# Optimization experiments

Measured on AMD Instinct MI355X. Metric: run time of the kernel, lower is better.

The kernel has to match this reference:

```python
import jax, jax.numpy as jnp
import numpy as np

PATCH, WIN = 3, 7


def _unfold(x, k):
    # torch F.unfold(x, k, padding=k//2), stride 1 -> [b, c, k*k, h, w]
    # channel-major ordering (c slowest, then kernel row, then kernel col)
    pad = k // 2
    b, c, h, w = x.shape
    xp = jnp.pad(x, ((0, 0), (0, 0), (pad, pad), (pad, pad)))
    return jnp.stack([xp[:, :, i:i + h, j:j + w]
                      for i in range(k) for j in range(k)], axis=2)


def _conv3(x, w, b=None):
    y = jax.lax.conv_general_dilated(x, w, (1, 1), [(1, 1), (1, 1)],
                                     dimension_numbers=('NCHW', 'OIHW', 'NCHW'))
    if b is not None:
        y = y + b[None, :, None, None]
    return y


def _head(u_feat, pan_feat, w_phi, w_theta, w_g, p, ws):
    # SelfAttention: windowed/patch neighborhood attention
    b, c, h, w = pan_feat.shape
    phi = jnp.einsum('oi,bihw->bohw', w_phi, pan_feat)
    theta = jnp.einsum('oi,bihw->bohw', w_theta, pan_feat)
    thp = _unfold(theta, p).reshape(b, c * p * p, h, w)        # [b,D,h,w]
    php = _unfold(phi, p).reshape(b, c * p * p, h, w)          # [b,D,h,w]
    phw = _unfold(php, ws)                                     # [b,D,K,h,w], K=ws*ws
    att = jax.nn.softmax(jnp.einsum('bdhw,bdkhw->bhwk', thp, phw), axis=-1)
    g = jnp.einsum('oi,bihw->bohw', w_g, u_feat)
    gw = _unfold(g, ws)                                        # [b,cu,K,h,w]
    return jnp.einsum('bhwk,bckhw->bchw', att, gw)


def _forward(u, pan, w_nlu, w_nlpan, g_phi, g_theta, g_g, s_phi, s_theta, s_g,
             m_phi, m_theta, m_g, mlp_w, mlp_b, w_resu, w_respan,
             rb0_w1, rb0_b1, rb0_w2, rb0_b2, rb1_w1, rb1_b1, rb1_w2, rb1_b2,
             rb2_w1, rb2_b1, rb2_w2, rb2_b2, w_recon):
    uf = _conv3(u, w_nlu)      # [b,5,h,w]
    pf = _conv3(pan, w_nlpan)  # [b,3,h,w]
    h1 = _head(uf, pf, g_phi, g_theta, g_g, PATCH, WIN)
    h2 = _head(uf, uf, s_phi, s_theta, s_g, 1, WIN)
    h3 = _head(uf, jnp.concatenate([uf, pf], axis=1), m_phi, m_theta, m_g, PATCH, WIN)
    # mlp: Linear(3,1) over stacked heads (last dim of size 3)
    att = h1 * mlp_w[0, 0] + h2 * mlp_w[0, 1] + h3 * mlp_w[0, 2] + mlp_b[0]
    ru = _conv3(u, w_resu)
    rp = _conv3(pan, w_respan)
    x = jnp.concatenate([att, ru, rp], axis=1)  # [b, fc+10, h, w]
    rbs = [(rb0_w1, rb0_b1, rb0_w2, rb0_b2),
           (rb1_w1, rb1_b1, rb1_w2, rb1_b2),
           (rb2_w1, rb2_b1, rb2_w2, rb2_b2)]
    for w1, b1, w2, b2 in rbs:
        f = jax.nn.relu(_conv3(x, w1, b1))
        f = _conv3(f, w2, b2)
        x = jax.nn.relu(f + x)
    return _conv3(x, w_recon)


def setup_inputs() -> dict:
    key = jax.random.key(0)
    ks = jax.random.split(key, 32)
    def n(i, shape, s=0.1):
        return jax.random.normal(ks[i], shape, dtype=jnp.float32) * s
    B, H, W = 1, 128, 128
    FC = 32
    C = FC + 10
    inp = {
        'u': jax.random.normal(ks[0], (B, 8, H, W), dtype=jnp.float32),
        'pan': jax.random.normal(ks[1], (B, 1, H, W), dtype=jnp.float32),
        'w_nlu': n(2, (5, 8, 3, 3)),
        'w_nlpan': n(3, (3, 1, 3, 3)),
        'g_phi': n(4, (3, 3)), 'g_theta': n(5, (3, 3)), 'g_g': n(6, (5, 5)),
        's_phi': n(7, (5, 5)), 's_theta': n(8, (5, 5)), 's_g': n(9, (5, 5)),
        'm_phi': n(10, (8, 8)), 'm_theta': n(11, (8, 8)), 'm_g': n(12, (5, 5)),
        'mlp_w': n(13, (1, 3), 0.5), 'mlp_b': n(14, (1,), 0.1),
        'w_resu': n(15, (FC, 8, 3, 3)), 'w_respan': n(16, (5, 1, 3, 3)),
        'w_recon': n(17, (8, C, 3, 3)),
    }
    k = 18
    for i in range(3):
        inp[f'rb{i}_w1'] = n(k, (C, C, 3, 3))
        inp[f'rb{i}_b1'] = n(k + 1, (C,), 0.01)
        inp[f'rb{i}_w2'] = n(k + 2, (C, C, 3, 3))
        inp[f'rb{i}_b2'] = n(k + 3, (C,), 0.01)
        k += 4
    return inp


def reference(u, pan, w_nlu, w_nlpan, g_phi, g_theta, g_g, s_phi, s_theta, s_g,
              m_phi, m_theta, m_g, mlp_w, mlp_b, w_resu, w_respan,
              rb0_w1, rb0_b1, rb0_w2, rb0_b2, rb1_w1, rb1_b1, rb1_w2, rb1_b2,
              rb2_w1, rb2_b1, rb2_w2, rb2_b2, w_recon):
    return _forward(u, pan, w_nlu, w_nlpan, g_phi, g_theta, g_g, s_phi, s_theta,
                    s_g, m_phi, m_theta, m_g, mlp_w, mlp_b, w_resu, w_respan,
                    rb0_w1, rb0_b1, rb0_w2, rb0_b2, rb1_w1, rb1_b1, rb1_w2,
                    rb1_b2, rb2_w1, rb2_b1, rb2_w2, rb2_b2, w_recon)
```

## Files before the change

kernel.cpp:

```cpp
#include <hip/hip_runtime.h>


#define DEV __device__ __forceinline__
typedef float f32x4 __attribute__((ext_vector_type(4)));
typedef __bf16 bf16x8 __attribute__((ext_vector_type(8)));
typedef unsigned short u16;
typedef unsigned int u32;

constexpr int N = 128 * 128;

constexpr int OFF_PHI1 =   0 * N;
constexpr int OFF_TH1  =   3 * N;
constexpr int OFF_PHI2 =   6 * N;
constexpr int OFF_TH2  =  11 * N;
constexpr int OFF_PHI3 =  16 * N;
constexpr int OFF_TH3  =  24 * N;
constexpr int OFF_G1   =  32 * N;
constexpr int OFF_G2   =  37 * N;
constexpr int OFF_G3   =  42 * N;
constexpr int OFF_X    =  47 * N;
constexpr int OFF_OH1  =  89 * N;
constexpr int OFF_OH2  =  94 * N;
constexpr int OFF_OH3  =  99 * N;
constexpr int XPLANE   = 130 * 136;
constexpr int OFF_XPAD = 110 * N;
constexpr int OFF_FPAD = 133 * N;
constexpr int OFF_SLAB = 156 * N;
constexpr int OFF_BTAB = 160 * N;
constexpr int SLAB_RB  = 18432;
constexpr int SLAB_RC  = 110592;
constexpr int SLAB_TOT = 116736;
constexpr int ZPB      = 528;
constexpr int ZTOT     = 2 * 42 * ZPB;
constexpr int WPREP_TOT = 384 + SLAB_TOT + ZTOT;

DEV bool inb(int y, int x) { return (unsigned)y < 128u && (unsigned)x < 128u; }
DEV u16 f2bf(float f) {
    unsigned u = __float_as_uint(f);
    return (u16)((u + 0x7fffu + ((u >> 16) & 1u)) >> 16);
}

__global__ __launch_bounds__(256, 2) void features_k(
    const float* __restrict__ u, const float* __restrict__ pan,
    const float* __restrict__ wnlu, const float* __restrict__ wnlpan,
    const float* __restrict__ gphi, const float* __restrict__ gth,
    const float* __restrict__ gg, const float* __restrict__ sphi,
    const float* __restrict__ sth, const float* __restrict__ sg,
    const float* __restrict__ mphi, const float* __restrict__ mth,
    const float* __restrict__ mg, float* __restrict__ ws) {
    const int p = blockIdx.x * 256 + threadIdx.x;
    const int y = p >> 7, x = p & 127;

    float uv[8][9];
#pragma unroll
    for (int ic = 0; ic < 8; ++ic)
#pragma unroll
        for (int i = 0; i < 3; ++i)
#pragma unroll
            for (int j = 0; j < 3; ++j) {
                int yy = y + i - 1, xx = x + j - 1;
                uv[ic][i * 3 + j] = inb(yy, xx) ? u[ic * N + yy * 128 + xx] : 0.f;
            }

    float uf[5] = {0, 0, 0, 0, 0};
#pragma unroll
    for (int ic = 0; ic < 8; ++ic)
#pragma unroll
        for (int k = 0; k < 9; ++k)
#pragma unroll
            for (int o = 0; o < 5; ++o)
                uf[o] = fmaf(uv[ic][k], wnlu[(o * 8 + ic) * 9 + k], uf[o]);

    if (blockIdx.y == 0) {
#pragma unroll
        for (int o = 0; o < 5; ++o) {
            float a = 0, b = 0, c1 = 0, c2 = 0, c3 = 0;
#pragma unroll
            for (int i = 0; i < 5; ++i) {
                a  = fmaf(sphi[o * 5 + i], uf[i], a);
                b  = fmaf(sth [o * 5 + i], uf[i], b);
                c1 = fmaf(gg  [o * 5 + i], uf[i], c1);
                c2 = fmaf(sg  [o * 5 + i], uf[i], c2);
                c3 = fmaf(mg  [o * 5 + i], uf[i], c3);
            }
            ws[OFF_PHI2 + o * N + p] = a;
            ws[OFF_TH2  + o * N + p] = b;
            ws[OFF_G1   + o * N + p] = c1;
            ws[OFF_G2   + o * N + p] = c2;
            ws[OFF_G3   + o * N + p] = c3;
        }
    } else {
        float pv[9];
#pragma unroll
        for (int i = 0; i < 3; ++i)
#pragma unroll
            for (int j = 0; j < 3; ++j) {
                int yy = y + i - 1, xx = x + j - 1;
                pv[i * 3 + j] = inb(yy, xx) ? pan[yy * 128 + xx] : 0.f;
            }
        float pf[3] = {0, 0, 0};
#pragma unroll
        for (int k = 0; k < 9; ++k)
#pragma unroll
            for (int o = 0; o < 3; ++o)
                pf[o] = fmaf(pv[k], wnlpan[o * 9 + k], pf[o]);

        float cat[8] = {uf[0], uf[1], uf[2], uf[3], uf[4], pf[0], pf[1], pf[2]};
#pragma unroll
        for (int o = 0; o < 3; ++o) {
            float a = 0, b = 0;
#pragma unroll
            for (int i = 0; i < 3; ++i) {
                a = fmaf(gphi[o * 3 + i], pf[i], a);
                b = fmaf(gth [o * 3 + i], pf[i], b);
            }
            ws[OFF_PHI1 + o * N + p] = a;
            ws[OFF_TH1  + o * N + p] = b;
        }
#pragma unroll
        for (int o = 0; o < 8; ++o) {
            float a = 0, b = 0;
#pragma unroll
            for (int i = 0; i < 8; ++i) {
                a = fmaf(mphi[o * 8 + i], cat[i], a);
                b = fmaf(mth [o * 8 + i], cat[i], b);
            }
            ws[OFF_PHI3 + o * N + p] = a;
            ws[OFF_TH3  + o * N + p] = b;
        }
    }
}

template <int C, int P>
DEV void head_tile(const float* __restrict__ phi, const float* __restrict__ theta,
                   const float* __restrict__ g, float* __restrict__ oh,
                   float* __restrict__ smem, int ty0, int tx0, int t) {
    constexpr int PR  = P / 2;
    constexpr int H3  = 3 + PR;
    constexpr int W   = 6 + P;
    constexpr int TTH = 8 + 2 * PR, TTW = 16 + 2 * PR;
    constexpr int PTH = 8 + 2 * H3, PTW = 16 + 2 * H3;
    constexpr int GTH = 14, GTW = 22;

    float* sT = smem;
    float* sP = sT + C * TTH * TTW;
    float* sG = sP + C * PTH * PTW;

#pragma unroll
    for (int c = 0; c < C; ++c)
#pragma unroll
        for (int base = 0; base < TTH * TTW; base += 256) {
            int i = base + t;
            if (i < TTH * TTW) {
                int r = i / TTW, cc = i - r * TTW;
                int gy = ty0 - PR + r, gx = tx0 - PR + cc;
                sT[c * TTH * TTW + i] =
                    inb(gy, gx) ? theta[c * N + gy * 128 + gx] : 0.f;
            }
        }
#pragma unroll
    for (int c = 0; c < C; ++c)
#pragma unroll
        for (int base = 0; base < PTH * PTW; base += 256) {
            int i = base + t;
            if (i < PTH * PTW) {
                int r = i / PTW, cc = i - r * PTW;
                int gy = ty0 - H3 + r, gx = tx0 - H3 + cc;
                sP[c * PTH * PTW + i] =
                    inb(gy, gx) ? phi[c * N + gy * 128 + gx] : 0.f;
            }
        }
#pragma unroll
    for (int c = 0; c < 5; ++c)
#pragma unroll
        for (int base = 0; base < GTH * GTW; base += 256) {
            int i = base + t;
            if (i < GTH * GTW) {
                int r = i / GTW, cc = i - r * GTW;
                int gy = ty0 - 3 + r, gx = tx0 - 3 + cc;
                sG[c * GTH * GTW + i] =
                    inb(gy, gx) ? g[c * N + gy * 128 + gx] : 0.f;
            }
        }
    __syncthreads();

    const int wave = t >> 6, lane = t & 63, m = lane >> 5;
    const int pidx = (lane & 31) | (wave << 5);
    const int py = pidx >> 4, px = pidx & 15;
    const int gy = ty0 + py, gx = tx0 + px;
    const int dbase = m * 3;

    float s[28];
#pragma unroll
    for (int k = 0; k < 28; ++k) s[k] = 0.f;

    for (int c = 0; c < C; ++c) {
        const float* tc = sT + c * TTH * TTW;
        const float* pc = sP + c * PTH * PTW;
        float T[P][P];
#pragma unroll
        for (int i = 0; i < P; ++i)
#pragma unroll
            for (int j = 0; j < P; ++j)
                T[i][j] = tc[(py + i) * TTW + px + j];
        float R[P][W];
#pragma unroll
        for (int r = 0; r < P; ++r)
#pragma unroll
            for (int w = 0; w < W; ++w)
                R[r][w] = pc[(py + dbase + r) * PTW + px + w];
#pragma unroll
        for (int dd = 0; dd < 4; ++dd) {
#pragma unroll
            for (int dx = 0; dx < 7; ++dx) {
                float a = 0.f;
#pragma unroll
                for (int i = 0; i < P; ++i)
#pragma unroll
                    for (int j = 0; j < P; ++j)
                        a = fmaf(T[i][j], R[i][dx + j], a);
                s[dd * 7 + dx] += a;
            }
            if (dd < 3) {
#pragma unroll
                for (int r = 0; r < P - 1; ++r)
#pragma unroll
                    for (int w = 0; w < W; ++w) R[r][w] = R[r + 1][w];
                int row = py + dbase + dd + P;
#pragma unroll
                for (int w = 0; w < W; ++w)
                    R[P - 1][w] = pc[row * PTW + px + w];
            }
        }
    }
#pragma unroll
    for (int k = 0; k < 28; ++k) {
        int d = dbase + k / 7, dx = k % 7;
        if (!inb(gy + d - 3, gx + dx - 3)) s[k] = 0.f;
    }
    const bool half0 = (m == 0);
    float mx = -3.0e38f;
#pragma unroll
    for (int k = 0; k < 28; ++k) {
        bool own = half0 || (k >= 7);
        mx = own ? fmaxf(mx, s[k]) : mx;
    }
    mx = fmaxf(mx, __shfl_xor(mx, 32));
    float sum = 0.f;
#pragma unroll
    for (int k = 0; k < 28; ++k) {
        bool own = half0 || (k >= 7);
        float e = own ? __expf(s[k] - mx) : 0.f;
        s[k] = e;
        sum += e;
    }
    sum += __shfl_xor(sum, 32);

    float o[5] = {0, 0, 0, 0, 0};
#pragma unroll
    for (int k = 0; k < 28; ++k) {
        int d = dbase + k / 7, dx = k % 7;
        int gr = (py + d) * GTW + px + dx;
#pragma unroll
        for (int c5 = 0; c5 < 5; ++c5)
            o[c5] = fmaf(s[k], sG[c5 * GTH * GTW + gr], o[c5]);
    }
#pragma unroll
    for (int c5 = 0; c5 < 5; ++c5) o[c5] += __shfl_xor(o[c5], 32);

    if (half0) {
        float inv = 1.f / sum;
        int p = gy * 128 + gx;
#pragma unroll
        for (int c5 = 0; c5 < 5; ++c5) oh[c5 * N + p] = o[c5] * inv;
    }
}

__global__ __launch_bounds__(256) void heads_k(float* __restrict__ ws) {
    __shared__ float smem[6052];
    const int t = threadIdx.x;
    const int ty0 = (blockIdx.x >> 3) * 8, tx0 = (blockIdx.x & 7) * 16;
    if (blockIdx.y == 0)
        head_tile<3, 3>(ws + OFF_PHI1, ws + OFF_TH1, ws + OFF_G1, ws + OFF_OH1,
                        smem, ty0, tx0, t);
    else if (blockIdx.y == 1)
        head_tile<5, 1>(ws + OFF_PHI2, ws + OFF_TH2, ws + OFF_G2, ws + OFF_OH2,
                        smem, ty0, tx0, t);
    else
        head_tile<8, 3>(ws + OFF_PHI3, ws + OFF_TH3, ws + OFF_G3, ws + OFF_OH3,
                        smem, ty0, tx0, t);
}

struct WPtrs { const float* w[7]; };

__global__ __launch_bounds__(256) void wprep_k(WPtrs wp, u16* __restrict__ slab,
                                               u16* __restrict__ btab,
                                               u16* __restrict__ xpad,
                                               u16* __restrict__ fpad) {
    int idx = blockIdx.x * 256 + threadIdx.x;
    if (idx >= WPREP_TOT) return;
    if (idx < 384) {
        u16 v = 0;
        if (idx < 378) {
            int ic = idx / 9, tau = idx - ic * 9;
            v = (u16)(ic * 216 + (tau / 3) * 72 + (tau % 3));
        }
        btab[idx] = v;
        return;
    }
    idx -= 384;
    if (idx < SLAB_TOT) {
        const float* W;
        int mt, ks, lane, j, ocv;
        if (idx < SLAB_RC) {
            int cv = idx / SLAB_RB, r = idx - cv * SLAB_RB;
            mt = r / 6144; r -= mt * 6144;
            ks = r / 512;  r -= ks * 512;
            lane = r / 8;  j = r - lane * 8;
            W = wp.w[cv]; ocv = 42;
        } else {
            int r = idx - SLAB_RC;
            mt = 0;
            ks = r / 512;  r -= ks * 512;
            lane = r / 8;  j = r - lane * 8;
            W = wp.w[6]; ocv = 8;
        }
        int k  = ks * 32 + (lane >> 4) * 8 + j;
        int oc = mt * 16 + (lane & 15);
        u16 v = 0;
        if (k < 378 && oc < ocv) {
            int ic = k / 9, tau = k - ic * 9;
            v = f2bf(W[(oc * 42 + ic) * 9 + tau]);
        }
        slab[idx] = v;
        return;
    }
    idx -= SLAB_TOT;
    u16* buf = (idx < 42 * ZPB) ? xpad : fpad;
    int e = (idx < 42 * ZPB) ? idx : idx - 42 * ZPB;
    int plane = e / ZPB, rem = e - plane * ZPB;
    int row, col;
    if (rem < 136)      { row = 0;             col = rem; }
    else if (rem < 272) { row = 129;           col = rem - 136; }
    else if (rem < 400) { row = 1 + rem - 272; col = 0; }
    else                { row = 1 + rem - 400; col = 129; }
    buf[plane * XPLANE + row * 136 + col] = 0;
}

__global__ __launch_bounds__(256, 2) void assemble_k(
    const float* __restrict__ u, const float* __restrict__ pan,
    const float* __restrict__ wres, const float* __restrict__ wrp,
    const float* __restrict__ mlpw, const float* __restrict__ mlpb,
    float* __restrict__ ws, u16* __restrict__ xpad) {
    const int p = blockIdx.x * 256 + threadIdx.x;
    const int y = p >> 7, x = p & 127;
    const int padp = (y + 1) * 136 + (x + 1);
    float* xb = ws + OFF_X;

    if (blockIdx.y == 0) {
        const float w0 = mlpw[0], w1 = mlpw[1], w2 = mlpw[2];
        const float bb = mlpb[0];
#pragma unroll
        for (int c = 0; c < 5; ++c) {
            float a = ws[OFF_OH1 + c * N + p] * w0 +
                      ws[OFF_OH2 + c * N + p] * w1 +
                      ws[OFF_OH3 + c * N + p] * w2 + bb;
            xb[c * N + p] = a;
            xpad[c * XPLANE + padp] = f2bf(a);
        }
        float pv[9];
#pragma unroll
        for (int i = 0; i < 3; ++i)
#pragma unroll
            for (int j = 0; j < 3; ++j) {
                int yy = y + i - 1, xx = x + j - 1;
                pv[i * 3 + j] = inb(yy, xx) ? pan[yy * 128 + xx] : 0.f;
            }
        float a5[5] = {0, 0, 0, 0, 0};
#pragma unroll
        for (int k = 0; k < 9; ++k)
#pragma unroll
            for (int o = 0; o < 5; ++o)
                a5[o] = fmaf(pv[k], wrp[o * 9 + k], a5[o]);
#pragma unroll
        for (int o = 0; o < 5; ++o) {
            xb[(37 + o) * N + p] = a5[o];
            xpad[(37 + o) * XPLANE + padp] = f2bf(a5[o]);
        }
    } else {
        const int ob = (blockIdx.y - 1) * 8;
        float uv[8][9];
#pragma unroll
        for (int ic = 0; ic < 8; ++ic)
#pragma unroll
            for (int i = 0; i < 3; ++i)
#pragma unroll
                for (int j = 0; j < 3; ++j) {
                    int yy = y + i - 1, xx = x + j - 1;
                    uv[ic][i * 3 + j] =
                        inb(yy, xx) ? u[ic * N + yy * 128 + xx] : 0.f;
                }
        float acc[8] = {0, 0, 0, 0, 0, 0, 0, 0};
#pragma unroll
        for (int ic = 0; ic < 8; ++ic)
#pragma unroll
            for (int k = 0; k < 9; ++k)
#pragma unroll
                for (int o = 0; o < 8; ++o)
                    acc[o] = fmaf(uv[ic][k], wres[((ob + o) * 8 + ic) * 9 + k],
                                  acc[o]);
#pragma unroll
        for (int o = 0; o < 8; ++o) {
            xb[(5 + ob + o) * N + p] = acc[o];
            xpad[(5 + ob + o) * XPLANE + padp] = f2bf(acc[o]);
        }
    }
}

template <int MT, int OCV, bool BIAS, bool RELU, bool SKIP, bool WF32, bool WPAD>
__global__ __launch_bounds__(256, 1) void convm_k(
    const u16* __restrict__ xin, const u16* __restrict__ slab,
    const u16* __restrict__ btab, const float* __restrict__ bs,
    const float* __restrict__ skip, float* __restrict__ of32,
    u16* __restrict__ opad) {
    __shared__ __align__(16) u16 sX[9072];
    __shared__ __align__(16) u16 sBt[384];
    const int t = threadIdx.x;
    const int y = blockIdx.x >> 1, x0 = (blockIdx.x & 1) << 6;

    const u16* srcbase = xin + y * 136 + x0;
#pragma unroll
    for (int it = 0; it < 4; ++it) {
        int c = it * 256 + t;
        if (c < 1008) {
            int row = c >> 3, slot = c & 7;
            int ic = row / 3, r = row - ic * 3;
            uint4 v = *((const uint4*)(srcbase + ic * XPLANE + r * 136) + slot);
            *(uint4*)(sX + row * 72 + slot * 8) = v;
        }
    }
    if (t < 126) {
        int ic = t / 3, r = t - ic * 3;
        u32 v = *(const u32*)(srcbase + ic * XPLANE + r * 136 + 64);
        *(u32*)(sX + t * 72 + 64) = v;
    }
    for (int i = t; i < 384; i += 256) sBt[i] = btab[i];
    __syncthreads();

    const int lane = t & 63, wave = t >> 6;
    const int quad = lane >> 4, col = lane & 15;
    const int ncol = wave * 16 + col;

    union AB { uint4 u; bf16x8 b; };
    AB a[MT][12];
#pragma unroll
    for (int mt = 0; mt < MT; ++mt)
#pragma unroll
        for (int ks = 0; ks < 12; ++ks)
            a[mt][ks].u = ((const uint4*)slab)[(mt * 12 + ks) * 64 + lane];

    f32x4 acc[MT];
#pragma unroll
    for (int mt = 0; mt < MT; ++mt) acc[mt] = {0.f, 0.f, 0.f, 0.f};

#pragma unroll
    for (int ks = 0; ks < 12; ++ks) {
        union { uint4 u; u16 s[8]; } off;
        off.u = *(const uint4*)(sBt + ks * 32 + quad * 8);
        union { u16 s[8]; bf16x8 b; } bv;
#pragma unroll
        for (int j = 0; j < 8; ++j) bv.s[j] = sX[off.s[j] + ncol];
#pragma unroll
        for (int mt = 0; mt < MT; ++mt)
            acc[mt] = __builtin_amdgcn_mfma_f32_16x16x32_bf16(
                a[mt][ks].b, bv.b, acc[mt], 0, 0, 0);
    }

    const int xg = x0 + ncol;
    const int px = y * 128 + xg;
    const int padp = (y + 1) * 136 + (xg + 1);
#pragma unroll
    for (int mt = 0; mt < MT; ++mt)
#pragma unroll
        for (int reg = 0; reg < 4; ++reg) {
            int oc = mt * 16 + quad * 4 + reg;
            if (oc < OCV) {
                float v = acc[mt][reg];
                if (BIAS) v += bs[oc];
                if (SKIP) v += skip[oc * N + px];
                if (RELU) v = fmaxf(v, 0.f);
                if (WF32) of32[oc * N + px] = v;
                if (WPAD) opad[oc * XPLANE + padp] = f2bf(v);
            }
        }
}

extern "C" void kernel_launch(void* const* d_in, const int* in_sizes, int n_in,
                              void* d_out, int out_size, void* d_ws, size_t ws_size,
                              hipStream_t stream) {
    (void)in_sizes; (void)n_in; (void)out_size; (void)ws_size;
    float* ws = (float*)d_ws;
    float* out = (float*)d_out;

    const float* u      = (const float*)d_in[0];
    const float* pan    = (const float*)d_in[1];
    const float* wnlu   = (const float*)d_in[2];
    const float* wnlpan = (const float*)d_in[3];
    const float* gphi   = (const float*)d_in[4];
    const float* gth    = (const float*)d_in[5];
    const float* gg     = (const float*)d_in[6];
    const float* sphi   = (const float*)d_in[7];
    const float* sth    = (const float*)d_in[8];
    const float* sg     = (const float*)d_in[9];
    const float* mphi   = (const float*)d_in[10];
    const float* mth    = (const float*)d_in[11];
    const float* mg     = (const float*)d_in[12];
    const float* mlpw   = (const float*)d_in[13];
    const float* mlpb   = (const float*)d_in[14];
    const float* wres   = (const float*)d_in[15];
    const float* wrp    = (const float*)d_in[16];
    const float* wrecon = (const float*)d_in[17];

    u16* xpad = (u16*)(ws + OFF_XPAD);
    u16* fpad = (u16*)(ws + OFF_FPAD);
    u16* slab = (u16*)(ws + OFF_SLAB);
    u16* btab = (u16*)(ws + OFF_BTAB);

    features_k<<<dim3(N / 256, 2), 256, 0, stream>>>(
        u, pan, wnlu, wnlpan, gphi, gth, gg, sphi, sth, sg, mphi, mth, mg, ws);
    heads_k<<<dim3(128, 3), 256, 0, stream>>>(ws);

    WPtrs wp;
    wp.w[0] = (const float*)d_in[18]; wp.w[1] = (const float*)d_in[20];
    wp.w[2] = (const float*)d_in[22]; wp.w[3] = (const float*)d_in[24];
    wp.w[4] = (const float*)d_in[26]; wp.w[5] = (const float*)d_in[28];
    wp.w[6] = wrecon;
    wprep_k<<<(WPREP_TOT + 255) / 256, 256, 0, stream>>>(wp, slab, btab,
                                                         xpad, fpad);

    assemble_k<<<dim3(N / 256, 5), 256, 0, stream>>>(u, pan, wres, wrp, mlpw,
                                                     mlpb, ws, xpad);

    for (int r = 0; r < 3; ++r) {
        const float* b1 = (const float*)d_in[19 + 4 * r];
        const float* b2 = (const float*)d_in[21 + 4 * r];
        convm_k<3, 42, true, true, false, false, true>
            <<<256, 256, 0, stream>>>(xpad, slab + (2 * r) * SLAB_RB, btab, b1,
                                      nullptr, nullptr, fpad);
        convm_k<3, 42, true, true, true, true, true>
            <<<256, 256, 0, stream>>>(fpad, slab + (2 * r + 1) * SLAB_RB, btab,
                                      b2, ws + OFF_X, ws + OFF_X, xpad);
    }
    convm_k<1, 8, false, false, false, true, false>
        <<<256, 256, 0, stream>>>(xpad, slab + SLAB_RC, btab, nullptr, nullptr,
                                  out, nullptr);
}
```

Measured before the change: 210.5 us.

## Merge feature and weight prep kernels, shrink head and conv tiles for more blocks

Folds the feature projection kernel and the weight/slab preparation kernel into one launch, with block ranges split by blockIdx. Head attention tiles shrink from 8x16 to 8x8 pixels with 128-thread blocks, giving 768 blocks instead of 384. The MFMA conv kernels go from 64-pixel to 32-pixel row segments with 128 threads and 512 blocks, and the shared row stride and gather table change to match. The aim is fewer launches and more blocks across the many CUs, at the cost of more halo reloading per pixel and less reuse.

```diff
diff --git a/kernel.cpp b/kernel.cpp
--- a/kernel.cpp
+++ b/kernel.cpp
@@ -33,6 +33,7 @@
 constexpr int ZPB      = 528;
 constexpr int ZTOT     = 2 * 42 * ZPB;
 constexpr int WPREP_TOT = 384 + SLAB_TOT + ZTOT;
+constexpr int WPREP_BLK = (WPREP_TOT + 255) / 256;
 
 DEV bool inb(int y, int x) { return (unsigned)y < 128u && (unsigned)x < 128u; }
 DEV u16 f2bf(float f) {
@@ -40,270 +41,112 @@
     return (u16)((u + 0x7fffu + ((u >> 16) & 1u)) >> 16);
 }
 
-__global__ __launch_bounds__(256, 2) void features_k(
-    const float* __restrict__ u, const float* __restrict__ pan,
-    const float* __restrict__ wnlu, const float* __restrict__ wnlpan,
-    const float* __restrict__ gphi, const float* __restrict__ gth,
-    const float* __restrict__ gg, const float* __restrict__ sphi,
-    const float* __restrict__ sth, const float* __restrict__ sg,
-    const float* __restrict__ mphi, const float* __restrict__ mth,
-    const float* __restrict__ mg, float* __restrict__ ws) {
-    const int p = blockIdx.x * 256 + threadIdx.x;
-    const int y = p >> 7, x = p & 127;
-
-    float uv[8][9];
-#pragma unroll
-    for (int ic = 0; ic < 8; ++ic)
-#pragma unroll
-        for (int i = 0; i < 3; ++i)
-#pragma unroll
-            for (int j = 0; j < 3; ++j) {
-                int yy = y + i - 1, xx = x + j - 1;
-                uv[ic][i * 3 + j] = inb(yy, xx) ? u[ic * N + yy * 128 + xx] : 0.f;
-            }
-
-    float uf[5] = {0, 0, 0, 0, 0};
-#pragma unroll
-    for (int ic = 0; ic < 8; ++ic)
-#pragma unroll
-        for (int k = 0; k < 9; ++k)
-#pragma unroll
-            for (int o = 0; o < 5; ++o)
-                uf[o] = fmaf(uv[ic][k], wnlu[(o * 8 + ic) * 9 + k], uf[o]);
-
-    if (blockIdx.y == 0) {
-#pragma unroll
-        for (int o = 0; o < 5; ++o) {
-            float a = 0, b = 0, c1 = 0, c2 = 0, c3 = 0;
-#pragma unroll
-            for (int i = 0; i < 5; ++i) {
-                a  = fmaf(sphi[o * 5 + i], uf[i], a);
-                b  = fmaf(sth [o * 5 + i], uf[i], b);
-                c1 = fmaf(gg  [o * 5 + i], uf[i], c1);
-                c2 = fmaf(sg  [o * 5 + i], uf[i], c2);
-                c3 = fmaf(mg  [o * 5 + i], uf[i], c3);
-            }
-            ws[OFF_PHI2 + o * N + p] = a;
-            ws[OFF_TH2  + o * N + p] = b;
-            ws[OFF_G1   + o * N + p] = c1;
-            ws[OFF_G2   + o * N + p] = c2;
-            ws[OFF_G3   + o * N + p] = c3;
-        }
-    } else {
-        float pv[9];
-#pragma unroll
-        for (int i = 0; i < 3; ++i)
-#pragma unroll
-            for (int j = 0; j < 3; ++j) {
-                int yy = y + i - 1, xx = x + j - 1;
-                pv[i * 3 + j] = inb(yy, xx) ? pan[yy * 128 + xx] : 0.f;
-            }
-        float pf[3] = {0, 0, 0};
-#pragma unroll
-        for (int k = 0; k < 9; ++k)
-#pragma unroll
-            for (int o = 0; o < 3; ++o)
-                pf[o] = fmaf(pv[k], wnlpan[o * 9 + k], pf[o]);
-
-        float cat[8] = {uf[0], uf[1], uf[2], uf[3], uf[4], pf[0], pf[1], pf[2]};
-#pragma unroll
-        for (int o = 0; o < 3; ++o) {
-            float a = 0, b = 0;
-#pragma unroll
-            for (int i = 0; i < 3; ++i) {
-                a = fmaf(gphi[o * 3 + i], pf[i], a);
-                b = fmaf(gth [o * 3 + i], pf[i], b);
-            }
-            ws[OFF_PHI1 + o * N + p] = a;
-            ws[OFF_TH1  + o * N + p] = b;
-        }
-#pragma unroll
-        for (int o = 0; o < 8; ++o) {
-            float a = 0, b = 0;
-#pragma unroll
-            for (int i = 0; i < 8; ++i) {
-                a = fmaf(mphi[o * 8 + i], cat[i], a);
-                b = fmaf(mth [o * 8 + i], cat[i], b);
-            }
-            ws[OFF_PHI3 + o * N + p] = a;
-            ws[OFF_TH3  + o * N + p] = b;
-        }
-    }
-}
-
-template <int C, int P>
-DEV void head_tile(const float* __restrict__ phi, const float* __restrict__ theta,
-                   const float* __restrict__ g, float* __restrict__ oh,
-                   float* __restrict__ smem, int ty0, int tx0, int t) {
-    constexpr int PR  = P / 2;
-    constexpr int H3  = 3 + PR;
-    constexpr int W   = 6 + P;
-    constexpr int TTH = 8 + 2 * PR, TTW = 16 + 2 * PR;
-    constexpr int PTH = 8 + 2 * H3, PTW = 16 + 2 * H3;
-    constexpr int GTH = 14, GTW = 22;
-
-    float* sT = smem;
-    float* sP = sT + C * TTH * TTW;
-    float* sG = sP + C * PTH * PTW;
-
-#pragma unroll
-    for (int c = 0; c < C; ++c)
-#pragma unroll
-        for (int base = 0; base < TTH * TTW; base += 256) {
-            int i = base + t;
-            if (i < TTH * TTW) {
-                int r = i / TTW, cc = i - r * TTW;
-                int gy = ty0 - PR + r, gx = tx0 - PR + cc;
-                sT[c * TTH * TTW + i] =
-                    inb(gy, gx) ? theta[c * N + gy * 128 + gx] : 0.f;
-            }
-        }
-#pragma unroll
-    for (int c = 0; c < C; ++c)
-#pragma unroll
-        for (int base = 0; base < PTH * PTW; base += 256) {
-            int i = base + t;
-            if (i < PTH * PTW) {
-                int r = i / PTW, cc = i - r * PTW;
-                int gy = ty0 - H3 + r, gx = tx0 - H3 + cc;
-                sP[c * PTH * PTW + i] =
-                    inb(gy, gx) ? phi[c * N + gy * 128 + gx] : 0.f;
-            }
-        }
-#pragma unroll
-    for (int c = 0; c < 5; ++c)
-#pragma unroll
-        for (int base = 0; base < GTH * GTW; base += 256) {
-            int i = base + t;
-            if (i < GTH * GTW) {
-                int r = i / GTW, cc = i - r * GTW;
-                int gy = ty0 - 3 + r, gx = tx0 - 3 + cc;
-                sG[c * GTH * GTW + i] =
-                    inb(gy, gx) ? g[c * N + gy * 128 + gx] : 0.f;
-            }
-        }
-    __syncthreads();
-
-    const int wave = t >> 6, lane = t & 63, m = lane >> 5;
-    const int pidx = (lane & 31) | (wave << 5);
-    const int py = pidx >> 4, px = pidx & 15;
-    const int gy = ty0 + py, gx = tx0 + px;
-    const int dbase = m * 3;
-
-    float s[28];
-#pragma unroll
-    for (int k = 0; k < 28; ++k) s[k] = 0.f;
-
-    for (int c = 0; c < C; ++c) {
-        const float* tc = sT + c * TTH * TTW;
-        const float* pc = sP + c * PTH * PTW;
-        float T[P][P];
-#pragma unroll
-        for (int i = 0; i < P; ++i)
-#pragma unroll
-            for (int j = 0; j < P; ++j)
-                T[i][j] = tc[(py + i) * TTW + px + j];
-        float R[P][W];
-#pragma unroll
-        for (int r = 0; r < P; ++r)
-#pragma unroll
-            for (int w = 0; w < W; ++w)
-                R[r][w] = pc[(py + dbase + r) * PTW + px + w];
-#pragma unroll
-        for (int dd = 0; dd < 4; ++dd) {
-#pragma unroll
-            for (int dx = 0; dx < 7; ++dx) {
-                float a = 0.f;
-#pragma unroll
-                for (int i = 0; i < P; ++i)
-#pragma unroll
-                    for (int j = 0; j < P; ++j)
-                        a = fmaf(T[i][j], R[i][dx + j], a);
-                s[dd * 7 + dx] += a;
-            }
-            if (dd < 3) {
-#pragma unroll
-                for (int r = 0; r < P - 1; ++r)
-#pragma unroll
-                    for (int w = 0; w < W; ++w) R[r][w] = R[r + 1][w];
-                int row = py + dbase + dd + P;
-#pragma unroll
-                for (int w = 0; w < W; ++w)
-                    R[P - 1][w] = pc[row * PTW + px + w];
-            }
-        }
-    }
-#pragma unroll
-    for (int k = 0; k < 28; ++k) {
-        int d = dbase + k / 7, dx = k % 7;
-        if (!inb(gy + d - 3, gx + dx - 3)) s[k] = 0.f;
-    }
-    const bool half0 = (m == 0);
-    float mx = -3.0e38f;
-#pragma unroll
-    for (int k = 0; k < 28; ++k) {
-        bool own = half0 || (k >= 7);
-        mx = own ? fmaxf(mx, s[k]) : mx;
-    }
-    mx = fmaxf(mx, __shfl_xor(mx, 32));
-    float sum = 0.f;
-#pragma unroll
-    for (int k = 0; k < 28; ++k) {
-        bool own = half0 || (k >= 7);
-        float e = own ? __expf(s[k] - mx) : 0.f;
-        s[k] = e;
-        sum += e;
-    }
-    sum += __shfl_xor(sum, 32);
-
-    float o[5] = {0, 0, 0, 0, 0};
-#pragma unroll
-    for (int k = 0; k < 28; ++k) {
-        int d = dbase + k / 7, dx = k % 7;
-        int gr = (py + d) * GTW + px + dx;
-#pragma unroll
-        for (int c5 = 0; c5 < 5; ++c5)
-            o[c5] = fmaf(s[k], sG[c5 * GTH * GTW + gr], o[c5]);
-    }
-#pragma unroll
-    for (int c5 = 0; c5 < 5; ++c5) o[c5] += __shfl_xor(o[c5], 32);
-
-    if (half0) {
-        float inv = 1.f / sum;
-        int p = gy * 128 + gx;
-#pragma unroll
-        for (int c5 = 0; c5 < 5; ++c5) oh[c5 * N + p] = o[c5] * inv;
-    }
-}
-
-__global__ __launch_bounds__(256) void heads_k(float* __restrict__ ws) {
-    __shared__ float smem[6052];
-    const int t = threadIdx.x;
-    const int ty0 = (blockIdx.x >> 3) * 8, tx0 = (blockIdx.x & 7) * 16;
-    if (blockIdx.y == 0)
-        head_tile<3, 3>(ws + OFF_PHI1, ws + OFF_TH1, ws + OFF_G1, ws + OFF_OH1,
-                        smem, ty0, tx0, t);
-    else if (blockIdx.y == 1)
-        head_tile<5, 1>(ws + OFF_PHI2, ws + OFF_TH2, ws + OFF_G2, ws + OFF_OH2,
-                        smem, ty0, tx0, t);
-    else
-        head_tile<8, 3>(ws + OFF_PHI3, ws + OFF_TH3, ws + OFF_G3, ws + OFF_OH3,
-                        smem, ty0, tx0, t);
-}
-
-struct WPtrs { const float* w[7]; };
-
-__global__ __launch_bounds__(256) void wprep_k(WPtrs wp, u16* __restrict__ slab,
-                                               u16* __restrict__ btab,
-                                               u16* __restrict__ xpad,
-                                               u16* __restrict__ fpad) {
-    int idx = blockIdx.x * 256 + threadIdx.x;
+struct PrepArgs {
+    const float* u;    const float* pan;  const float* wnlu; const float* wnlpan;
+    const float* gphi; const float* gth;  const float* gg;   const float* sphi;
+    const float* sth;  const float* sg;   const float* mphi; const float* mth;
+    const float* mg;
+    const float* w[7];
+};
+
+__global__ __launch_bounds__(256) void prep_k(PrepArgs pa, float* __restrict__ ws,
+                                              u16* __restrict__ slab,
+                                              u16* __restrict__ btab,
+                                              u16* __restrict__ xpad,
+                                              u16* __restrict__ fpad) {
+    const int bid = blockIdx.x, t = threadIdx.x;
+    if (bid < 128) {
+        const int p = (bid & 63) * 256 + t;
+        const int y = p >> 7, x = p & 127;
+
+        float uv[8][9];
+#pragma unroll
+        for (int ic = 0; ic < 8; ++ic)
+#pragma unroll
+            for (int i = 0; i < 3; ++i)
+#pragma unroll
+                for (int j = 0; j < 3; ++j) {
+                    int yy = y + i - 1, xx = x + j - 1;
+                    uv[ic][i * 3 + j] =
+                        inb(yy, xx) ? pa.u[ic * N + yy * 128 + xx] : 0.f;
+                }
+        float uf[5] = {0, 0, 0, 0, 0};
+#pragma unroll
+        for (int ic = 0; ic < 8; ++ic)
+#pragma unroll
+            for (int k = 0; k < 9; ++k)
+#pragma unroll
+                for (int o = 0; o < 5; ++o)
+                    uf[o] = fmaf(uv[ic][k], pa.wnlu[(o * 8 + ic) * 9 + k], uf[o]);
+
+        if (bid < 64) {
+#pragma unroll
+            for (int o = 0; o < 5; ++o) {
+                float a = 0, b = 0, c1 = 0, c2 = 0, c3 = 0;
+#pragma unroll
+                for (int i = 0; i < 5; ++i) {
+                    a  = fmaf(pa.sphi[o * 5 + i], uf[i], a);
+                    b  = fmaf(pa.sth [o * 5 + i], uf[i], b);
+                    c1 = fmaf(pa.gg  [o * 5 + i], uf[i], c1);
+                    c2 = fmaf(pa.sg  [o * 5 + i], uf[i], c2);
+                    c3 = fmaf(pa.mg  [o * 5 + i], uf[i], c3);
+                }
+                ws[OFF_PHI2 + o * N + p] = a;
+                ws[OFF_TH2  + o * N + p] = b;
+                ws[OFF_G1   + o * N + p] = c1;
+                ws[OFF_G2   + o * N + p] = c2;
+                ws[OFF_G3   + o * N + p] = c3;
+            }
+        } else {
+            float pv[9];
+#pragma unroll
+            for (int i = 0; i < 3; ++i)
+#pragma unroll
+                for (int j = 0; j < 3; ++j) {
+                    int yy = y + i - 1, xx = x + j - 1;
+                    pv[i * 3 + j] = inb(yy, xx) ? pa.pan[yy * 128 + xx] : 0.f;
+                }
+            float pf[3] = {0, 0, 0};
+#pragma unroll
+            for (int k = 0; k < 9; ++k)
+#pragma unroll
+                for (int o = 0; o < 3; ++o)
+                    pf[o] = fmaf(pv[k], pa.wnlpan[o * 9 + k], pf[o]);
+            float cat[8] = {uf[0], uf[1], uf[2], uf[3], uf[4],
+                            pf[0], pf[1], pf[2]};
+#pragma unroll
+            for (int o = 0; o < 3; ++o) {
+                float a = 0, b = 0;
+#pragma unroll
+                for (int i = 0; i < 3; ++i) {
+                    a = fmaf(pa.gphi[o * 3 + i], pf[i], a);
+                    b = fmaf(pa.gth [o * 3 + i], pf[i], b);
+                }
+                ws[OFF_PHI1 + o * N + p] = a;
+                ws[OFF_TH1  + o * N + p] = b;
+            }
+#pragma unroll
+            for (int o = 0; o < 8; ++o) {
+                float a = 0, b = 0;
+#pragma unroll
+                for (int i = 0; i < 8; ++i) {
+                    a = fmaf(pa.mphi[o * 8 + i], cat[i], a);
+                    b = fmaf(pa.mth [o * 8 + i], cat[i], b);
+                }
+                ws[OFF_PHI3 + o * N + p] = a;
+                ws[OFF_TH3  + o * N + p] = b;
+            }
+        }
+        return;
+    }
+
+    int idx = (bid - 128) * 256 + t;
     if (idx >= WPREP_TOT) return;
     if (idx < 384) {
         u16 v = 0;
         if (idx < 378) {
             int ic = idx / 9, tau = idx - ic * 9;
-            v = (u16)(ic * 216 + (tau / 3) * 72 + (tau % 3));
+            v = (u16)(ic * 120 + (tau / 3) * 40 + (tau % 3));
         }
         btab[idx] = v;
         return;
@@ -317,13 +160,13 @@
             mt = r / 6144; r -= mt * 6144;
             ks = r / 512;  r -= ks * 512;
             lane = r / 8;  j = r - lane * 8;
-            W = wp.w[cv]; ocv = 42;
+            W = pa.w[cv]; ocv = 42;
         } else {
             int r = idx - SLAB_RC;
             mt = 0;
             ks = r / 512;  r -= ks * 512;
             lane = r / 8;  j = r - lane * 8;
-            W = wp.w[6]; ocv = 8;
+            W = pa.w[6]; ocv = 8;
         }
         int k  = ks * 32 + (lane >> 4) * 8 + j;
         int oc = mt * 16 + (lane & 15);
@@ -347,6 +190,166 @@
     buf[plane * XPLANE + row * 136 + col] = 0;
 }
 
+template <int C, int P>
+DEV void head_tile(const float* __restrict__ phi, const float* __restrict__ theta,
+                   const float* __restrict__ g, float* __restrict__ oh,
+                   float* __restrict__ smem, int ty0, int tx0, int t) {
+    constexpr int PR  = P / 2;
+    constexpr int H3  = 3 + PR;
+    constexpr int W   = 6 + P;
+    constexpr int TTH = 8 + 2 * PR, TTW = 8 + 2 * PR;
+    constexpr int PTH = 8 + 2 * H3, PTW = 8 + 2 * H3;
+    constexpr int GTH = 14, GTW = 14;
+
+    float* sT = smem;
+    float* sP = sT + C * TTH * TTW;
+    float* sG = sP + C * PTH * PTW;
+
+#pragma unroll
+    for (int c = 0; c < C; ++c)
+#pragma unroll
+        for (int base = 0; base < TTH * TTW; base += 128) {
+            int i = base + t;
+            if (i < TTH * TTW) {
+                int r = i / TTW, cc = i - r * TTW;
+                int gy = ty0 - PR + r, gx = tx0 - PR + cc;
+                sT[c * TTH * TTW + i] =
+                    inb(gy, gx) ? theta[c * N + gy * 128 + gx] : 0.f;
+            }
+        }
+#pragma unroll
+    for (int c = 0; c < C; ++c)
+#pragma unroll
+        for (int base = 0; base < PTH * PTW; base += 128) {
+            int i = base + t;
+            if (i < PTH * PTW) {
+                int r = i / PTW, cc = i - r * PTW;
+                int gy = ty0 - H3 + r, gx = tx0 - H3 + cc;
+                sP[c * PTH * PTW + i] =
+                    inb(gy, gx) ? phi[c * N + gy * 128 + gx] : 0.f;
+            }
+        }
+#pragma unroll
+    for (int c = 0; c < 5; ++c)
+#pragma unroll
+        for (int base = 0; base < GTH * GTW; base += 128) {
+            int i = base + t;
+            if (i < GTH * GTW) {
+                int r = i / GTW, cc = i - r * GTW;
+                int gy = ty0 - 3 + r, gx = tx0 - 3 + cc;
+                sG[c * GTH * GTW + i] =
+                    inb(gy, gx) ? g[c * N + gy * 128 + gx] : 0.f;
+            }
+        }
+    __syncthreads();
+
+    const int wave = t >> 6, lane = t & 63, m = lane >> 5;
+    const int pidx = (lane & 31) | (wave << 5);
+    const int py = pidx >> 3, px = pidx & 7;
+    const int gy = ty0 + py, gx = tx0 + px;
+    const int dbase = m * 3;
+
+    float s[28];
+#pragma unroll
+    for (int k = 0; k < 28; ++k) s[k] = 0.f;
+
+    for (int c = 0; c < C; ++c) {
+        const float* tc = sT + c * TTH * TTW;
+        const float* pc = sP + c * PTH * PTW;
+        float T[P][P];
+#pragma unroll
+        for (int i = 0; i < P; ++i)
+#pragma unroll
+            for (int j = 0; j < P; ++j)
+                T[i][j] = tc[(py + i) * TTW + px + j];
+        float R[P][W];
+#pragma unroll
+        for (int r = 0; r < P; ++r)
+#pragma unroll
+            for (int w = 0; w < W; ++w)
+                R[r][w] = pc[(py + dbase + r) * PTW + px + w];
+#pragma unroll
+        for (int dd = 0; dd < 4; ++dd) {
+#pragma unroll
+            for (int dx = 0; dx < 7; ++dx) {
+                float a = 0.f;
+#pragma unroll
+                for (int i = 0; i < P; ++i)
+#pragma unroll
+                    for (int j = 0; j < P; ++j)
+                        a = fmaf(T[i][j], R[i][dx + j], a);
+                s[dd * 7 + dx] += a;
+            }
+            if (dd < 3) {
+#pragma unroll
+                for (int r = 0; r < P - 1; ++r)
+#pragma unroll
+                    for (int w = 0; w < W; ++w) R[r][w] = R[r + 1][w];
+                int row = py + dbase + dd + P;
+#pragma unroll
+                for (int w = 0; w < W; ++w)
+                    R[P - 1][w] = pc[row * PTW + px + w];
+            }
+        }
+    }
+#pragma unroll
+    for (int k = 0; k < 28; ++k) {
+        int d = dbase + k / 7, dx = k % 7;
+        if (!inb(gy + d - 3, gx + dx - 3)) s[k] = 0.f;
+    }
+    const bool half0 = (m == 0);
+    float mx = -3.0e38f;
+#pragma unroll
+    for (int k = 0; k < 28; ++k) {
+        bool own = half0 || (k >= 7);
+        mx = own ? fmaxf(mx, s[k]) : mx;
+    }
+    mx = fmaxf(mx, __shfl_xor(mx, 32));
+    float sum = 0.f;
+#pragma unroll
+    for (int k = 0; k < 28; ++k) {
+        bool own = half0 || (k >= 7);
+        float e = own ? __expf(s[k] - mx) : 0.f;
+        s[k] = e;
+        sum += e;
+    }
+    sum += __shfl_xor(sum, 32);
+
+    float o[5] = {0, 0, 0, 0, 0};
+#pragma unroll
+    for (int k = 0; k < 28; ++k) {
+        int d = dbase + k / 7, dx = k % 7;
+        int gr = (py + d) * GTW + px + dx;
+#pragma unroll
+        for (int c5 = 0; c5 < 5; ++c5)
+            o[c5] = fmaf(s[k], sG[c5 * GTH * GTW + gr], o[c5]);
+    }
+#pragma unroll
+    for (int c5 = 0; c5 < 5; ++c5) o[c5] += __shfl_xor(o[c5], 32);
+
+    if (half0) {
+        float inv = 1.f / sum;
+        int p = gy * 128 + gx;
+#pragma unroll
+        for (int c5 = 0; c5 < 5; ++c5) oh[c5 * N + p] = o[c5] * inv;
+    }
+}
+
+__global__ __launch_bounds__(128) void heads_k(float* __restrict__ ws) {
+    __shared__ float smem[3828];
+    const int t = threadIdx.x;
+    const int ty0 = (blockIdx.x >> 4) * 8, tx0 = (blockIdx.x & 15) * 8;
+    if (blockIdx.y == 0)
+        head_tile<3, 3>(ws + OFF_PHI1, ws + OFF_TH1, ws + OFF_G1, ws + OFF_OH1,
+                        smem, ty0, tx0, t);
+    else if (blockIdx.y == 1)
+        head_tile<5, 1>(ws + OFF_PHI2, ws + OFF_TH2, ws + OFF_G2, ws + OFF_OH2,
+                        smem, ty0, tx0, t);
+    else
+        head_tile<8, 3>(ws + OFF_PHI3, ws + OFF_TH3, ws + OFF_G3, ws + OFF_OH3,
+                        smem, ty0, tx0, t);
+}
+
 __global__ __launch_bounds__(256, 2) void assemble_k(
     const float* __restrict__ u, const float* __restrict__ pan,
     const float* __restrict__ wres, const float* __restrict__ wrp,
@@ -418,33 +421,29 @@
 }
 
 template <int MT, int OCV, bool BIAS, bool RELU, bool SKIP, bool WF32, bool WPAD>
-__global__ __launch_bounds__(256, 1) void convm_k(
+__global__ __launch_bounds__(128, 1) void convm_k(
     const u16* __restrict__ xin, const u16* __restrict__ slab,
     const u16* __restrict__ btab, const float* __restrict__ bs,
     const float* __restrict__ skip, float* __restrict__ of32,
     u16* __restrict__ opad) {
-    __shared__ __align__(16) u16 sX[9072];
+    __shared__ __align__(16) u16 sX[5040];
     __shared__ __align__(16) u16 sBt[384];
     const int t = threadIdx.x;
-    const int y = blockIdx.x >> 1, x0 = (blockIdx.x & 1) << 6;
+    const int y = blockIdx.x >> 2, x0 = (blockIdx.x & 3) << 5;
 
     const u16* srcbase = xin + y * 136 + x0;
 #pragma unroll
-    for (int it = 0; it < 4; ++it) {
-        int c = it * 256 + t;
-        if (c < 1008) {
-            int row = c >> 3, slot = c & 7;
+    for (int it = 0; it < 5; ++it) {
+        int c = it * 128 + t;
+        if (c < 630) {
+            int row = c / 5, slot = c - row * 5;
             int ic = row / 3, r = row - ic * 3;
             uint4 v = *((const uint4*)(srcbase + ic * XPLANE + r * 136) + slot);
-            *(uint4*)(sX + row * 72 + slot * 8) = v;
-        }
-    }
-    if (t < 126) {
-        int ic = t / 3, r = t - ic * 3;
-        u32 v = *(const u32*)(srcbase + ic * XPLANE + r * 136 + 64);
-        *(u32*)(sX + t * 72 + 64) = v;
-    }
-    for (int i = t; i < 384; i += 256) sBt[i] = btab[i];
+            *(uint4*)(sX + row * 40 + slot * 8) = v;
+        }
+    }
+#pragma unroll
+    for (int it = 0; it < 3; ++it) sBt[it * 128 + t] = btab[it * 128 + t];
     __syncthreads();
 
     const int lane = t & 63, wave = t >> 6;
@@ -502,56 +501,54 @@
     float* ws = (float*)d_ws;
     float* out = (float*)d_out;
 
-    const float* u      = (const float*)d_in[0];
-    const float* pan    = (const float*)d_in[1];
-    const float* wnlu   = (const float*)d_in[2];
-    const float* wnlpan = (const float*)d_in[3];
-    const float* gphi   = (const float*)d_in[4];
-    const float* gth    = (const float*)d_in[5];
-    const float* gg     = (const float*)d_in[6];
-    const float* sphi   = (const float*)d_in[7];
-    const float* sth    = (const float*)d_in[8];
-    const float* sg     = (const float*)d_in[9];
-    const float* mphi   = (const float*)d_in[10];
-    const float* mth    = (const float*)d_in[11];
-    const float* mg     = (const float*)d_in[12];
-    const float* mlpw   = (const float*)d_in[13];
-    const float* mlpb   = (const float*)d_in[14];
-    const float* wres   = (const float*)d_in[15];
-    const float* wrp    = (const float*)d_in[16];
-    const float* wrecon = (const float*)d_in[17];
+    PrepArgs pa;
+    pa.u      = (const float*)d_in[0];
+    pa.pan    = (const float*)d_in[1];
+    pa.wnlu   = (const float*)d_in[2];
+    pa.wnlpan = (const float*)d_in[3];
+    pa.gphi   = (const float*)d_in[4];
+    pa.gth    = (const float*)d_in[5];
+    pa.gg     = (const float*)d_in[6];
+    pa.sphi   = (const float*)d_in[7];
+    pa.sth    = (const float*)d_in[8];
+    pa.sg     = (const float*)d_in[9];
+    pa.mphi   = (const float*)d_in[10];
+    pa.mth    = (const float*)d_in[11];
+    pa.mg     = (const float*)d_in[12];
+    pa.w[0]   = (const float*)d_in[18];
+    pa.w[1]   = (const float*)d_in[20];
+    pa.w[2]   = (const float*)d_in[22];
+    pa.w[3]   = (const float*)d_in[24];
+    pa.w[4]   = (const float*)d_in[26];
+    pa.w[5]   = (const float*)d_in[28];
+    pa.w[6]   = (const float*)d_in[17];
+
+    const float* mlpw = (const float*)d_in[13];
+    const float* mlpb = (const float*)d_in[14];
+    const float* wres = (const float*)d_in[15];
+    const float* wrp  = (const float*)d_in[16];
 
     u16* xpad = (u16*)(ws + OFF_XPAD);
     u16* fpad = (u16*)(ws + OFF_FPAD);
     u16* slab = (u16*)(ws + OFF_SLAB);
     u16* btab = (u16*)(ws + OFF_BTAB);
 
-    features_k<<<dim3(N / 256, 2), 256, 0, stream>>>(
-        u, pan, wnlu, wnlpan, gphi, gth, gg, sphi, sth, sg, mphi, mth, mg, ws);
-    heads_k<<<dim3(128, 3), 256, 0, stream>>>(ws);
-
-    WPtrs wp;
-    wp.w[0] = (const float*)d_in[18]; wp.w[1] = (const float*)d_in[20];
-    wp.w[2] = (const float*)d_in[22]; wp.w[3] = (const float*)d_in[24];
-    wp.w[4] = (const float*)d_in[26]; wp.w[5] = (const float*)d_in[28];
-    wp.w[6] = wrecon;
-    wprep_k<<<(WPREP_TOT + 255) / 256, 256, 0, stream>>>(wp, slab, btab,
-                                                         xpad, fpad);
-
-    assemble_k<<<dim3(N / 256, 5), 256, 0, stream>>>(u, pan, wres, wrp, mlpw,
-                                                     mlpb, ws, xpad);
+    prep_k<<<128 + WPREP_BLK, 256, 0, stream>>>(pa, ws, slab, btab, xpad, fpad);
+    heads_k<<<dim3(256, 3), 128, 0, stream>>>(ws);
+    assemble_k<<<dim3(64, 5), 256, 0, stream>>>(pa.u, pa.pan, wres, wrp, mlpw,
+                                                mlpb, ws, xpad);
 
     for (int r = 0; r < 3; ++r) {
         const float* b1 = (const float*)d_in[19 + 4 * r];
         const float* b2 = (const float*)d_in[21 + 4 * r];
         convm_k<3, 42, true, true, false, false, true>
-            <<<256, 256, 0, stream>>>(xpad, slab + (2 * r) * SLAB_RB, btab, b1,
+            <<<512, 128, 0, stream>>>(xpad, slab + (2 * r) * SLAB_RB, btab, b1,
                                       nullptr, nullptr, fpad);
         convm_k<3, 42, true, true, true, true, true>
-            <<<256, 256, 0, stream>>>(fpad, slab + (2 * r + 1) * SLAB_RB, btab,
+            <<<512, 128, 0, stream>>>(fpad, slab + (2 * r + 1) * SLAB_RB, btab,
                                       b2, ws + OFF_X, ws + OFF_X, xpad);
     }
     convm_k<1, 8, false, false, false, true, false>
-        <<<256, 256, 0, stream>>>(xpad, slab + SLAB_RC, btab, nullptr, nullptr,
+        <<<512, 128, 0, stream>>>(xpad, slab + SLAB_RC, btab, nullptr, nullptr,
                                   out, nullptr);
 }
```

After: 210.9 us. No clear change (+0.2%).
